# Kernel optimization log

Hardware: AMD Instinct MI355X
Metric: run time of the kernel (lower is better)

## Reference

```python
import jax, jax.numpy as jnp
import numpy as np

K = 3  # kernel size per dim
PAD = K // 2
CHANS = [1, 40, 80, 160, 80, 40, 1]  # channel ladder of the 6 convNd layers


def conv4d(x, w, b):
    """4D convolution, stride 1, 'same' padding.
    x: [B, Cin, D1, D2, D3, D4]; w: [Cout, Cin, K, K, K, K]; b: [Cout].
    Implemented as K shifted 3D convs along D1 (D1 folded into batch), summed.
    """
    B, Cin, D1, D2, D3, D4 = x.shape
    Cout = w.shape[0]
    # pad only D1 here; the inner conv pads D2..D4
    xp = jnp.pad(x, ((0, 0), (0, 0), (PAD, PAD), (0, 0), (0, 0), (0, 0)))
    xp = jnp.transpose(xp, (0, 2, 1, 3, 4, 5))  # [B, D1+2p, Cin, D2, D3, D4]
    dn = jax.lax.conv_dimension_numbers(
        (B * D1, Cin, D2, D3, D4), (Cout, Cin, K, K, K),
        ('NCDHW', 'OIDHW', 'NCDHW'))
    acc = None
    for i in range(K):  # small fixed loop over kernel taps along D1
        xs = xp[:, i:i + D1].reshape(B * D1, Cin, D2, D3, D4)
        y = jax.lax.conv_general_dilated(
            xs, w[:, :, i], window_strides=(1, 1, 1),
            padding=[(PAD, PAD)] * 3, dimension_numbers=dn)
        acc = y if acc is None else acc + y
    out = acc.reshape(B, D1, Cout, D2, D3, D4)
    out = jnp.transpose(out, (0, 2, 1, 3, 4, 5))
    return out + b[None, :, None, None, None, None]


def setup_inputs() -> dict:
    key = jax.random.key(0)
    kx, key = jax.random.split(key)
    inp = {'x': jax.random.normal(kx, (2, 1, 16, 16, 16, 16), dtype=jnp.float32)}
    for l in range(6):
        kw, key = jax.random.split(key)
        cin, cout = CHANS[l], CHANS[l + 1]
        std = (2.0 / (cin * K ** 4)) ** 0.5  # Kaiming-style fan-in init
        inp[f'w{l + 1}'] = jax.random.normal(kw, (cout, cin, K, K, K, K), dtype=jnp.float32) * std
        inp[f'b{l + 1}'] = jnp.zeros((cout,), dtype=jnp.float32)
    return inp


def reference(x, w1, b1, w2, b2, w3, b3, w4, b4, w5, b5, w6, b6):
    h = jax.nn.relu(conv4d(x, w1, b1))
    h = jax.nn.relu(conv4d(h, w2, b2))
    h = jax.nn.relu(conv4d(h, w3, b3))
    h = jax.nn.relu(conv4d(h, w4, b4))
    h = jax.nn.relu(conv4d(h, w5, b5))
    h = conv4d(h, w6, b6)
    return jax.nn.relu(h)
```

## Files before the change

kernel.cpp:

```cpp
#include <hip/hip_runtime.h>

typedef __attribute__((ext_vector_type(8))) short short8;
typedef __attribute__((ext_vector_type(4))) float f32x4;

__device__ __forceinline__ ushort f2bf(float f){
    union { float f; unsigned u; } v; v.f = f;
    unsigned r = (v.u + 0x7fffu + ((v.u >> 16) & 1u)) >> 16;
    return (ushort)r;
}
__device__ __forceinline__ float bf2f(ushort u){
    union { unsigned u; float f; } v; v.u = ((unsigned)u) << 16;
    return v.f;
}

__global__ __launch_bounds__(256) void conv_l1(
    const float* __restrict__ x, const float* __restrict__ w,
    const float* __restrict__ bias, ushort* __restrict__ out)
{
    __shared__ float xs[2916];
    __shared__ float wsh[3240];
    const int tid = threadIdx.x;
    const int bx = blockIdx.x;
    const int d2 = bx & 15, d1 = (bx >> 4) & 15, b = bx >> 8;
    const float* xb = x + (size_t)b * 65536;

    for (int i = tid; i < 2916; i += 256){
        int i4 = i % 18; int r1 = i / 18; int i3 = r1 % 18;
        int r2 = r1 / 18; int a2 = r2 % 3; int a1 = r2 / 3;
        int e1 = d1 + a1 - 1, e2 = d2 + a2 - 1, e3 = i3 - 1, e4 = i4 - 1;
        float v = 0.f;
        if ((unsigned)e1 < 16u && (unsigned)e2 < 16u && (unsigned)e3 < 16u && (unsigned)e4 < 16u)
            v = xb[((e1 * 16 + e2) * 16 + e3) * 16 + e4];
        xs[i] = v;
    }
    for (int i = tid; i < 3240; i += 256) wsh[i] = w[i];
    __syncthreads();

    const int d3 = tid >> 4, d4 = tid & 15;
    float acc[40];
    #pragma unroll
    for (int c = 0; c < 40; ++c) acc[c] = 0.f;

    for (int t1 = 0; t1 < 3; ++t1)
    for (int t2 = 0; t2 < 3; ++t2)
    for (int t3 = 0; t3 < 3; ++t3)
    #pragma unroll
    for (int t4 = 0; t4 < 3; ++t4){
        float xv = xs[((t1 * 3 + t2) * 18 + d3 + t3) * 18 + d4 + t4];
        int tap = ((t1 * 3 + t2) * 3 + t3) * 3 + t4;
        #pragma unroll
        for (int c = 0; c < 40; ++c) acc[c] += wsh[c * 81 + tap] * xv;
    }

    ushort* ob = out + ((size_t)bx * 256 + tid) * 64;
    #pragma unroll
    for (int c = 0; c < 40; ++c){
        float v = acc[c] + bias[c]; v = v > 0.f ? v : 0.f;
        ob[c] = f2bf(v);
    }
    #pragma unroll
    for (int c = 40; c < 64; ++c) ob[c] = 0;
}

__global__ __launch_bounds__(256) void conv_l6(
    const ushort* __restrict__ in, const float* __restrict__ w,
    const float* __restrict__ bias, float* __restrict__ out)
{
    __shared__ float wsh[3240];
    const int tid = threadIdx.x;
    const int bx = blockIdx.x;
    const int d2 = bx & 15, d1 = (bx >> 4) & 15, b = bx >> 8;
    for (int i = tid; i < 3240; i += 256) wsh[i] = w[i];
    __syncthreads();

    const int d3 = tid >> 4, d4 = tid & 15;
    const ushort* inb = in + (size_t)b * 65536 * 48;
    float acc = 0.f;
    for (int t1 = 0; t1 < 3; ++t1){
        int e1 = d1 + t1 - 1; if ((unsigned)e1 >= 16u) continue;
        for (int t2 = 0; t2 < 3; ++t2){
            int e2 = d2 + t2 - 1; if ((unsigned)e2 >= 16u) continue;
            for (int t3 = 0; t3 < 3; ++t3){
                int e3 = d3 + t3 - 1; if ((unsigned)e3 >= 16u) continue;
                for (int t4 = 0; t4 < 3; ++t4){
                    int e4 = d4 + t4 - 1; if ((unsigned)e4 >= 16u) continue;
                    const ushort* p = inb + (size_t)(((e1 * 16 + e2) * 16 + e3) * 16 + e4) * 48;
                    int tap = ((t1 * 3 + t2) * 3 + t3) * 3 + t4;
                    #pragma unroll
                    for (int c8 = 0; c8 < 5; ++c8){
                        short8 v = *(const short8*)(p + c8 * 8);
                        #pragma unroll
                        for (int j = 0; j < 8; ++j)
                            acc += bf2f((ushort)v[j]) * wsh[(c8 * 8 + j) * 81 + tap];
                    }
                }
            }
        }
    }
    float v = acc + bias[0]; v = v > 0.f ? v : 0.f;
    out[(size_t)bx * 256 + tid] = v;
}

__global__ void repack_w(const float* __restrict__ w, ushort* __restrict__ wp,
                         int cin, int cout, int cin_s, int cout_c)
{
    const int total = 81 * cin_s * cout_c;
    for (int i = blockIdx.x * blockDim.x + threadIdx.x; i < total; i += gridDim.x * blockDim.x){
        int j = i & 7;
        int rest = i >> 3;
        int co = rest % cout_c;
        int rest2 = rest / cout_c;
        int ci_hi = rest2 % (cin_s >> 3);
        int t = rest2 / (cin_s >> 3);
        int ci = ci_hi * 8 + j;
        float v = (ci < cin && co < cout) ? w[((size_t)co * cin + ci) * 81 + t] : 0.f;
        wp[i] = f2bf(v);
    }
}

template<int CIN_S, int COUT_W, int COUT_TOT, int OST, int CREAL, int PADC>
__global__ __launch_bounds__(256, 2) void conv16(
    const ushort* __restrict__ in, const ushort* __restrict__ wp,
    const float* __restrict__ bias, ushort* __restrict__ out)
{
    constexpr int KC   = CIN_S / 32;
    constexpr int NT   = COUT_W / 16;
    constexpr int A8   = 1024;
    constexpr int NLA  = A8 / 256;
    constexpr int B8   = 12 * COUT_W;
    constexpr int NLB  = (B8 + 255) / 256;

    __shared__ __attribute__((aligned(16))) ushort As[2][8192];
    __shared__ __attribute__((aligned(16))) ushort Bs[2][B8 * 8];

    const int tid  = threadIdx.x;
    const int lane = tid & 63;
    const int wm   = tid >> 6;
    const int r    = lane & 15;
    const int g    = lane >> 4;

    const int p0 = blockIdx.x;
    const int strip = p0 >> 9;
    const int pp = p0 & 511;
    const int bx = (pp & 7) * 64 + (pp >> 3);
    const int d2 = bx & 15, d1 = (bx >> 4) & 15, b = bx >> 8;
    const int co_base = strip * COUT_W;

    const ushort* inb = in + (size_t)b * 65536 * CIN_S;

    unsigned long long gpack = 0ull; int ng = 0;
    #pragma unroll
    for (int gg = 0; gg < 9; ++gg){
        const int t1 = gg / 3, t2 = gg - (gg / 3) * 3;
        if ((unsigned)(d1 + t1 - 1) < 16u && (unsigned)(d2 + t2 - 1) < 16u){
            gpack |= ((unsigned long long)gg) << (ng * 4);
            ++ng;
        }
    }
    const int nchunk = ng * KC;
    const int nstep  = nchunk * 3;

    f32x4 acc[4][NT];
    #pragma unroll
    for (int mi = 0; mi < 4; ++mi)
        #pragma unroll
        for (int n = 0; n < NT; ++n)
            acc[mi][n] = (f32x4){0.f, 0.f, 0.f, 0.f};

    short8 areg[NLA];
    short8 brg0[NLB], brg1[NLB];

    auto loadAreg = [&](int c){
        const int gi = c / KC, kh = c - gi * KC;
        const int gg = (int)((gpack >> (gi * 4)) & 15ull);
        const int t1 = gg / 3, t2 = gg - t1 * 3;
        const ushort* src = inb + ((size_t)((d1 + t1 - 1) * 16 + (d2 + t2 - 1)) * 256) * CIN_S + kh * 32;
        #pragma unroll
        for (int k = 0; k < NLA; ++k){
            const int i = tid + k * 256;
            areg[k] = *(const short8*)(src + (size_t)(i >> 2) * CIN_S + (i & 3) * 8);
        }
    };
    auto writeA = [&](ushort* dst){
        #pragma unroll
        for (int k = 0; k < NLA; ++k){
            const int i = tid + k * 256;
            const int pos = i >> 2, gc = i & 3;
            const int gs = gc ^ ((pos >> 1) & 3);
            *(short8*)(dst + pos * 32 + gs * 8) = areg[k];
        }
    };
    auto loadBreg = [&](int s, short8 (&brg)[NLB]){
        const int c = s / 3, t3 = s - c * 3;
        const int gi = c / KC, kh = c - gi * KC;
        const int gg = (int)((gpack >> (gi * 4)) & 15ull);
        const int tap0 = gg * 9 + t3 * 3;
        #pragma unroll
        for (int k = 0; k < NLB; ++k){
            const int i = tid + k * 256;
            if (i < B8){
                const int t4 = i / (4 * COUT_W);
                const int rest = i - t4 * (4 * COUT_W);
                const int gk = rest / COUT_W;
                const int col = rest - gk * COUT_W;
                brg[k] = *((const short8*)wp +
                           ((size_t)(tap0 + t4) * (CIN_S / 8) + kh * 4 + gk) * COUT_TOT + co_base + col);
            }
        }
    };
    auto writeB = [&](ushort* dst, short8 (&brg)[NLB]){
        #pragma unroll
        for (int k = 0; k < NLB; ++k){
            const int i = tid + k * 256;
            if (i < B8){
                const int gk = (i / COUT_W) & 3;
                *(short8*)(dst + ((i * 8) ^ (gk << 3))) = brg[k];
            }
        }
    };

    loadAreg(0);
    loadBreg(0, brg0);
    writeA(As[0]);
    writeB(Bs[0], brg0);
    if (nchunk > 1) loadAreg(1);
    if (nstep > 1) loadBreg(1, brg1);
    __syncthreads();

    int c = 0, t3 = 0;
    for (int s = 0; s < nstep; ++s){
        if (s + 1 < nstep){
            if ((s + 1) & 1) writeB(Bs[1], brg1); else writeB(Bs[0], brg0);
        }
        if (t3 == 0 && c + 1 < nchunk) writeA(As[(c + 1) & 1]);
        if (t3 == 1 && c + 2 < nchunk) loadAreg(c + 2);
        if (s + 2 < nstep){
            if (s & 1) loadBreg(s + 2, brg1); else loadBreg(s + 2, brg0);
        }

        const ushort* Ab = As[c & 1];
        const ushort* Bb = Bs[s & 1];
        __builtin_amdgcn_s_setprio(1);
        #pragma unroll
        for (int t4 = 0; t4 < 3; ++t4){
            const int e4 = r + t4 - 1;
            const bool v4 = (unsigned)e4 < 16u;
            const int gsw = (g ^ ((e4 >> 1) & 3)) << 3;
            short8 bfr[NT];
            #pragma unroll
            for (int n = 0; n < NT; ++n)
                bfr[n] = *(const short8*)(Bb + ((((t4 * 4 + g) * COUT_W + n * 16 + r) * 8) ^ (g << 3)));
            #pragma unroll
            for (int mi = 0; mi < 4; ++mi){
                const int e3 = 4 * wm + mi + t3 - 1;
                short8 af = {0, 0, 0, 0, 0, 0, 0, 0};
                if (v4 && (unsigned)e3 < 16u)
                    af = *(const short8*)(Ab + (e3 * 16 + e4) * 32 + gsw);
                #pragma unroll
                for (int n = 0; n < NT; ++n)
                    acc[mi][n] = __builtin_amdgcn_mfma_f32_16x16x32_bf16(af, bfr[n], acc[mi][n], 0, 0, 0);
            }
        }
        __builtin_amdgcn_s_setprio(0);

        asm volatile("s_waitcnt lgkmcnt(0)" ::: "memory");
        __builtin_amdgcn_s_barrier();
        __builtin_amdgcn_sched_barrier(0);

        ++t3; if (t3 == 3){ t3 = 0; ++c; }
    }

    float bv[NT];
    #pragma unroll
    for (int n = 0; n < NT; ++n){
        const int co = co_base + n * 16 + r;
        bv[n] = (co < CREAL) ? bias[co] : 0.f;
    }
    ushort* ob = out + (size_t)bx * 256 * OST;
    #pragma unroll
    for (int mi = 0; mi < 4; ++mi){
        #pragma unroll
        for (int n = 0; n < NT; ++n){
            const int co = co_base + n * 16 + r;
            #pragma unroll
            for (int j = 0; j < 4; ++j){
                const int row = 64 * wm + 16 * mi + g * 4 + j;
                float v = acc[mi][n][j] + bv[n];
                v = v > 0.f ? v : 0.f;
                ob[(size_t)row * OST + co] = f2bf(v);
            }
        }
    }
    if (PADC > 0){
        const int row = 64 * wm + lane;
        const short8 z = {0, 0, 0, 0, 0, 0, 0, 0};
        #pragma unroll
        for (int pc = 0; pc < PADC; pc += 8)
            *(short8*)(ob + (size_t)row * OST + CREAL + pc) = z;
    }
}

extern "C" void kernel_launch(void* const* d_in, const int* in_sizes, int n_in,
                              void* d_out, int out_size, void* d_ws, size_t ws_size,
                              hipStream_t stream) {
    const float* x  = (const float*)d_in[0];
    const float* w1 = (const float*)d_in[1];  const float* b1 = (const float*)d_in[2];
    const float* w2 = (const float*)d_in[3];  const float* b2 = (const float*)d_in[4];
    const float* w3 = (const float*)d_in[5];  const float* b3 = (const float*)d_in[6];
    const float* w4 = (const float*)d_in[7];  const float* b4 = (const float*)d_in[8];
    const float* w5 = (const float*)d_in[9];  const float* b5 = (const float*)d_in[10];
    const float* w6 = (const float*)d_in[11]; const float* b6 = (const float*)d_in[12];

    ushort* bufA = (ushort*)d_ws;
    ushort* bufB = bufA + (size_t)131072 * 160;
    ushort* wp2  = bufB + (size_t)131072 * 96;
    ushort* wp3  = wp2 + (size_t)81 * 64 * 80;
    ushort* wp4  = wp3 + (size_t)81 * 96 * 160;
    ushort* wp5  = wp4 + (size_t)81 * 160 * 80;

    repack_w<<<512, 256, 0, stream>>>(w2, wp2, 40, 80, 64, 80);
    repack_w<<<512, 256, 0, stream>>>(w3, wp3, 80, 160, 96, 160);
    repack_w<<<512, 256, 0, stream>>>(w4, wp4, 160, 80, 160, 80);
    repack_w<<<512, 256, 0, stream>>>(w5, wp5, 80, 40, 96, 48);

    conv_l1<<<512, 256, 0, stream>>>(x, w1, b1, bufA);
    conv16<  64,   80,  80,  96,  80,  16><<< 512, 256, 0, stream>>>(bufA, wp2, b2, bufB);
    conv16<  96,   80, 160, 160, 160,   0><<<1024, 256, 0, stream>>>(bufB, wp3, b3, bufA);
    conv16< 160,   80,  80,  96,  80,  16><<< 512, 256, 0, stream>>>(bufA, wp4, b4, bufB);
    conv16<  96,   48,  48,  48,  40,   0><<< 512, 256, 0, stream>>>(bufB, wp5, b5, bufA);
    conv_l6<<<512, 256, 0, stream>>>(bufA, w6, b6, (float*)d_out);
}
```

Measured before the change: 993.5 us.

## Load conv tiles directly into LDS and pre-swizzle weights per step

Result: faster. 871.7 us (-12.3%).

```diff
diff --git a/kernel.cpp b/kernel.cpp
--- a/kernel.cpp
+++ b/kernel.cpp
@@ -2,6 +2,10 @@
 
 typedef __attribute__((ext_vector_type(8))) short short8;
 typedef __attribute__((ext_vector_type(4))) float f32x4;
+
+#define GLD16(gsrc, ldst) __builtin_amdgcn_global_load_lds( \
+    (const __attribute__((address_space(1))) unsigned int*)(gsrc), \
+    (__attribute__((address_space(3))) unsigned int*)(ldst), 16, 0, 0)
 
 __device__ __forceinline__ ushort f2bf(float f){
     union { float f; unsigned u; } v; v.f = f;
@@ -101,37 +105,51 @@
     out[(size_t)bx * 256 + tid] = v;
 }
 
-__global__ void repack_w(const float* __restrict__ w, ushort* __restrict__ wp,
-                         int cin, int cout, int cin_s, int cout_c)
+__global__ void repack_wq(const float* __restrict__ w, ushort* __restrict__ wq,
+                          int cin_real, int cout_real, int kc, int cout_w, int nstrip)
 {
-    const int total = 81 * cin_s * cout_c;
-    for (int i = blockIdx.x * blockDim.x + threadIdx.x; i < total; i += gridDim.x * blockDim.x){
-        int j = i & 7;
-        int rest = i >> 3;
-        int co = rest % cout_c;
-        int rest2 = rest / cout_c;
-        int ci_hi = rest2 % (cin_s >> 3);
-        int t = rest2 / (cin_s >> 3);
-        int ci = ci_hi * 8 + j;
-        float v = (ci < cin && co < cout) ? w[((size_t)co * cin + ci) * 81 + t] : 0.f;
-        wp[i] = f2bf(v);
-    }
-}
-
-template<int CIN_S, int COUT_W, int COUT_TOT, int OST, int CREAL, int PADC>
+    const int ncc = 27 * kc;
+    const int total = nstrip * ncc * 8192;
+    for (int o = blockIdx.x * blockDim.x + threadIdx.x; o < total; o += gridDim.x * blockDim.x){
+        const int j = o & 7;
+        const int u_phys = (o >> 3) & 1023;
+        const int chunk = o >> 13;
+        const int strip = chunk / ncc;
+        const int cc = chunk - strip * ncc;
+        const int gg = cc / (kc * 3);
+        const int rem = cc - gg * (kc * 3);
+        const int kh = rem / 3;
+        const int t3 = rem - kh * 3;
+        float v = 0.f;
+        if (u_phys < 12 * cout_w){
+            const int per = 4 * cout_w;
+            const int gk = ((u_phys % per) / cout_w) & 3;
+            const int u = u_phys ^ gk;
+            const int t4 = u / per;
+            const int rest = u - t4 * per;
+            const int gk2 = rest / cout_w;
+            const int col = rest - gk2 * cout_w;
+            const int tap = gg * 9 + t3 * 3 + t4;
+            const int ci = kh * 32 + gk2 * 8 + j;
+            const int co = strip * cout_w + col;
+            if (ci < cin_real && co < cout_real)
+                v = w[((size_t)co * cin_real + ci) * 81 + tap];
+        }
+        wq[o] = f2bf(v);
+    }
+}
+
+template<int CIN_S, int COUT_W, int OST, int CREAL, int PADC>
 __global__ __launch_bounds__(256, 2) void conv16(
-    const ushort* __restrict__ in, const ushort* __restrict__ wp,
+    const ushort* __restrict__ in, const ushort* __restrict__ wq,
     const float* __restrict__ bias, ushort* __restrict__ out)
 {
-    constexpr int KC   = CIN_S / 32;
-    constexpr int NT   = COUT_W / 16;
-    constexpr int A8   = 1024;
-    constexpr int NLA  = A8 / 256;
-    constexpr int B8   = 12 * COUT_W;
-    constexpr int NLB  = (B8 + 255) / 256;
+    constexpr int KC  = CIN_S / 32;
+    constexpr int NT  = COUT_W / 16;
+    constexpr int NCC = 27 * KC;
 
     __shared__ __attribute__((aligned(16))) ushort As[2][8192];
-    __shared__ __attribute__((aligned(16))) ushort Bs[2][B8 * 8];
+    __shared__ __attribute__((aligned(16))) ushort Bs[2][8192];
 
     const int tid  = threadIdx.x;
     const int lane = tid & 63;
@@ -147,6 +165,7 @@
     const int co_base = strip * COUT_W;
 
     const ushort* inb = in + (size_t)b * 65536 * CIN_S;
+    const ushort* wqs = wq + ((size_t)strip * NCC << 13);
 
     unsigned long long gpack = 0ull; int ng = 0;
     #pragma unroll
@@ -167,76 +186,51 @@
         for (int n = 0; n < NT; ++n)
             acc[mi][n] = (f32x4){0.f, 0.f, 0.f, 0.f};
 
-    short8 areg[NLA];
-    short8 brg0[NLB], brg1[NLB];
-
-    auto loadAreg = [&](int c){
-        const int gi = c / KC, kh = c - gi * KC;
+    const int ubase = (tid >> 6) * 256;
+    const int ul = tid & 63;
+
+    auto issueB = [&](int sn, ushort* dst){
+        const int cc = sn / 3, tt = sn - cc * 3;
+        const int gi = cc / KC, kh = cc - gi * KC;
+        const int gg = (int)((gpack >> (gi * 4)) & 15ull);
+        const ushort* src = wqs + ((size_t)((gg * KC + kh) * 3 + tt) << 13);
+        #pragma unroll
+        for (int k = 0; k < 4; ++k){
+            const int u0 = ubase + k * 64;
+            GLD16(src + (size_t)(u0 + ul) * 8, dst + u0 * 8);
+        }
+    };
+    auto issueA = [&](int cn, ushort* dst){
+        const int gi = cn / KC, kh = cn - gi * KC;
         const int gg = (int)((gpack >> (gi * 4)) & 15ull);
         const int t1 = gg / 3, t2 = gg - t1 * 3;
         const ushort* src = inb + ((size_t)((d1 + t1 - 1) * 16 + (d2 + t2 - 1)) * 256) * CIN_S + kh * 32;
         #pragma unroll
-        for (int k = 0; k < NLA; ++k){
-            const int i = tid + k * 256;
-            areg[k] = *(const short8*)(src + (size_t)(i >> 2) * CIN_S + (i & 3) * 8);
+        for (int k = 0; k < 4; ++k){
+            const int u0 = ubase + k * 64;
+            const int u = u0 + ul;
+            const int pos = u >> 2;
+            const int gc = (u & 3) ^ ((u >> 3) & 3);
+            GLD16(src + (size_t)pos * CIN_S + gc * 8, dst + u0 * 8);
         }
     };
-    auto writeA = [&](ushort* dst){
-        #pragma unroll
-        for (int k = 0; k < NLA; ++k){
-            const int i = tid + k * 256;
-            const int pos = i >> 2, gc = i & 3;
-            const int gs = gc ^ ((pos >> 1) & 3);
-            *(short8*)(dst + pos * 32 + gs * 8) = areg[k];
-        }
-    };
-    auto loadBreg = [&](int s, short8 (&brg)[NLB]){
-        const int c = s / 3, t3 = s - c * 3;
-        const int gi = c / KC, kh = c - gi * KC;
-        const int gg = (int)((gpack >> (gi * 4)) & 15ull);
-        const int tap0 = gg * 9 + t3 * 3;
-        #pragma unroll
-        for (int k = 0; k < NLB; ++k){
-            const int i = tid + k * 256;
-            if (i < B8){
-                const int t4 = i / (4 * COUT_W);
-                const int rest = i - t4 * (4 * COUT_W);
-                const int gk = rest / COUT_W;
-                const int col = rest - gk * COUT_W;
-                brg[k] = *((const short8*)wp +
-                           ((size_t)(tap0 + t4) * (CIN_S / 8) + kh * 4 + gk) * COUT_TOT + co_base + col);
-            }
-        }
-    };
-    auto writeB = [&](ushort* dst, short8 (&brg)[NLB]){
-        #pragma unroll
-        for (int k = 0; k < NLB; ++k){
-            const int i = tid + k * 256;
-            if (i < B8){
-                const int gk = (i / COUT_W) & 3;
-                *(short8*)(dst + ((i * 8) ^ (gk << 3))) = brg[k];
-            }
-        }
-    };
-
-    loadAreg(0);
-    loadBreg(0, brg0);
-    writeA(As[0]);
-    writeB(Bs[0], brg0);
-    if (nchunk > 1) loadAreg(1);
-    if (nstep > 1) loadBreg(1, brg1);
-    __syncthreads();
+
+    issueA(0, As[0]);
+    issueB(0, Bs[0]);
+    asm volatile("s_waitcnt vmcnt(0)" ::: "memory");
+    __builtin_amdgcn_s_barrier();
+    __builtin_amdgcn_sched_barrier(0);
 
     int c = 0, t3 = 0;
     for (int s = 0; s < nstep; ++s){
-        if (s + 1 < nstep){
-            if ((s + 1) & 1) writeB(Bs[1], brg1); else writeB(Bs[0], brg0);
-        }
-        if (t3 == 0 && c + 1 < nchunk) writeA(As[(c + 1) & 1]);
-        if (t3 == 1 && c + 2 < nchunk) loadAreg(c + 2);
-        if (s + 2 < nstep){
-            if (s & 1) loadBreg(s + 2, brg1); else loadBreg(s + 2, brg0);
-        }
+        int nis = 0;
+        if (s + 1 < nstep){ issueB(s + 1, Bs[(s + 1) & 1]); nis += 4; }
+        if (t3 == 0 && c + 1 < nchunk){ issueA(c + 1, As[(c + 1) & 1]); nis += 4; }
+        if (nis == 8)      asm volatile("s_waitcnt vmcnt(8)" ::: "memory");
+        else if (nis == 4) asm volatile("s_waitcnt vmcnt(4)" ::: "memory");
+        else               asm volatile("s_waitcnt vmcnt(0)" ::: "memory");
+        __builtin_amdgcn_s_barrier();
+        __builtin_amdgcn_sched_barrier(0);
 
         const ushort* Ab = As[c & 1];
         const ushort* Bb = Bs[s & 1];
@@ -263,7 +257,7 @@
         }
         __builtin_amdgcn_s_setprio(0);
 
-        asm volatile("s_waitcnt lgkmcnt(0)" ::: "memory");
+        __builtin_amdgcn_sched_barrier(0);
         __builtin_amdgcn_s_barrier();
         __builtin_amdgcn_sched_barrier(0);
 
@@ -313,20 +307,20 @@
 
     ushort* bufA = (ushort*)d_ws;
     ushort* bufB = bufA + (size_t)131072 * 160;
-    ushort* wp2  = bufB + (size_t)131072 * 96;
-    ushort* wp3  = wp2 + (size_t)81 * 64 * 80;
-    ushort* wp4  = wp3 + (size_t)81 * 96 * 160;
-    ushort* wp5  = wp4 + (size_t)81 * 160 * 80;
-
-    repack_w<<<512, 256, 0, stream>>>(w2, wp2, 40, 80, 64, 80);
-    repack_w<<<512, 256, 0, stream>>>(w3, wp3, 80, 160, 96, 160);
-    repack_w<<<512, 256, 0, stream>>>(w4, wp4, 160, 80, 160, 80);
-    repack_w<<<512, 256, 0, stream>>>(w5, wp5, 80, 40, 96, 48);
+    ushort* wq2  = bufB + (size_t)131072 * 96;
+    ushort* wq3  = wq2 + (size_t)54  * 8192;
+    ushort* wq4  = wq3 + (size_t)162 * 8192;
+    ushort* wq5  = wq4 + (size_t)135 * 8192;
+
+    repack_wq<<<512, 256, 0, stream>>>(w2, wq2,  40,  80, 2, 80, 1);
+    repack_wq<<<512, 256, 0, stream>>>(w3, wq3,  80, 160, 3, 80, 2);
+    repack_wq<<<512, 256, 0, stream>>>(w4, wq4, 160,  80, 5, 80, 1);
+    repack_wq<<<512, 256, 0, stream>>>(w5, wq5,  80,  40, 3, 48, 1);
 
     conv_l1<<<512, 256, 0, stream>>>(x, w1, b1, bufA);
-    conv16<  64,   80,  80,  96,  80,  16><<< 512, 256, 0, stream>>>(bufA, wp2, b2, bufB);
-    conv16<  96,   80, 160, 160, 160,   0><<<1024, 256, 0, stream>>>(bufB, wp3, b3, bufA);
-    conv16< 160,   80,  80,  96,  80,  16><<< 512, 256, 0, stream>>>(bufA, wp4, b4, bufB);
-    conv16<  96,   48,  48,  48,  40,   0><<< 512, 256, 0, stream>>>(bufB, wp5, b5, bufA);
+    conv16<  64,   80,  96,  80,  16><<< 512, 256, 0, stream>>>(bufA, wq2, b2, bufB);
+    conv16<  96,   80, 160, 160,   0><<<1024, 256, 0, stream>>>(bufB, wq3, b3, bufA);
+    conv16< 160,   80,  96,  80,  16><<< 512, 256, 0, stream>>>(bufA, wq4, b4, bufB);
+    conv16<  96,   48,  48,  40,   0><<< 512, 256, 0, stream>>>(bufB, wq5, b5, bufA);
     conv_l6<<<512, 256, 0, stream>>>(bufA, w6, b6, (float*)d_out);
 }
```
